# Kernel tuning notes

Measured on AMD Instinct MI355X. Metric: run time of the kernel, lower is better.

Reference implementation:

```python
import jax, jax.numpy as jnp
import numpy as np

B, N, FD = 8, 32768, 32
NUM_GROUP, GROUP_SIZE = 1024, 32
RAD_FIVE_DEG = 0.087266  # radians_of_five_degrees threshold


def setup_inputs() -> dict:
    key = jax.random.key(0)
    k1, k2, k3 = jax.random.split(key, 3)
    coord = jax.random.normal(k1, (B * N, 3), dtype=jnp.float32)
    feat = jax.random.normal(k2, (B * N, FD), dtype=jnp.float32)
    labels = jax.random.randint(k3, (B * N,), 0, 20)
    offset = jnp.cumsum(jnp.full((B,), N, dtype=jnp.int32))  # [N, 2N, ..., BN]
    return {"coord": coord, "feat": feat, "labels": labels, "offset": offset}


def _fps(coords, num_samples):
    """Farthest point sampling on one cloud. coords: [N,3] -> [num_samples] indices."""
    d = jnp.sum((coords - coords[0]) ** 2, axis=-1)  # dist to first selected point

    def step(dist, _):
        idx = jnp.argmax(dist)
        nd = jnp.sum((coords - coords[idx]) ** 2, axis=-1)
        return jnp.minimum(dist, nd), idx

    _, idxs = jax.lax.scan(step, d, None, length=num_samples - 1)
    return jnp.concatenate([jnp.zeros((1,), dtype=idxs.dtype), idxs])


def reference(coord, feat, labels, offset):
    b = offset.shape[0]
    n = coord.shape[0] // b
    c = coord.reshape(b, n, 3)        # [B,N,3]
    f = feat.reshape(b, n, FD)        # [B,N,FD]
    lab = labels.reshape(b, n)

    # --- FPS: num_group samples per cloud ---
    s_idx = jax.vmap(_fps, in_axes=(0, None))(c, NUM_GROUP)  # [B,G]

    s_xyz = jnp.take_along_axis(c, s_idx[..., None], axis=1)          # [B,G,3]
    s_feat = jnp.take_along_axis(f, s_idx[..., None], axis=1)         # [B,G,FD]
    s_labels = jnp.take_along_axis(lab, s_idx, axis=1)                # [B,G]

    # --- kNN within each cloud: [B,G,N] distance matrix, top-k smallest ---
    d2 = jnp.sum((s_xyz[:, :, None, :] - c[:, None, :, :]) ** 2, axis=-1)  # [B,G,N]
    _, n_idx = jax.lax.top_k(-d2, GROUP_SIZE)                              # [B,G,K] ascending distance

    # gather neighbor features: [B,G,K,FD]
    s_n_feat = jax.vmap(lambda fb, ib: fb[ib])(f, n_idx)

    # --- point curvature: 2*atan2(||a*|b| - |a|*b||, ||a*|b| + |a|*b||) ---
    a = s_feat[:, :, None, :]                                   # [B,G,1,FD]
    an = jnp.linalg.norm(a, axis=-1, keepdims=True)             # [B,G,1,1]
    bn = jnp.linalg.norm(s_n_feat, axis=-1, keepdims=True)      # [B,G,K,1]
    num = jnp.linalg.norm(a * bn - an * s_n_feat, axis=-1)      # [B,G,K]
    den = jnp.linalg.norm(a * bn + an * s_n_feat, axis=-1)      # [B,G,K]
    angles = 2.0 * jnp.arctan2(num, den)                        # [B,G,K]
    # drop self neighbor (first, distance 0), mean over remaining
    p_curv = jnp.mean(angles[:, :, 1:], axis=-1, keepdims=True)  # [B,G,1]

    shape_weight = (p_curv > RAD_FIVE_DEG).astype(jnp.int32).squeeze(-1)  # [B,G]
    feat_out = jnp.concatenate([s_feat, p_curv], axis=-1)                 # [B,G,FD+1]

    # flat index back to parent (global flat indexing, per original flat layout)
    s_idx_flat = s_idx + jnp.arange(b, dtype=s_idx.dtype)[:, None] * n

    return (s_xyz.reshape(-1, 3),
            feat_out.reshape(-1, FD + 1),
            shape_weight.reshape(-1),
            s_labels.reshape(-1),
            s_idx_flat.reshape(-1))
```

## Files before the change

### kernel.cpp

```cpp
#include <hip/hip_runtime.h>
#include <math.h>

#define BATCH   8
#define NPTS    32768
#define FDIM    32
#define NGROUP  1024
#define GSIZE   32
#define KLANE   8

#define NBLK    8
#define FTPB    512
#define CHUNK   (NPTS / NBLK)
#define NFPSBLK (BATCH * NBLK)
#define KNNQPB  8
#define NKNNBLK ((BATCH * NGROUP) / KNNQPB)

__device__ __forceinline__ float dist2f(float ax, float ay, float az,
                                        float bx, float by, float bz) {
  float dx = __fsub_rn(ax, bx);
  float dy = __fsub_rn(ay, by);
  float dz = __fsub_rn(az, bz);
  return __fadd_rn(__fadd_rn(__fmul_rn(dx, dx), __fmul_rn(dy, dy)),
                   __fmul_rn(dz, dz));
}

#define X8(M) M(0) M(1) M(2) M(3) M(4) M(5) M(6) M(7)

__global__ __launch_bounds__(FTPB) void fused_kernel(
    const float* __restrict__ coord, const float* __restrict__ feat,
    const int* __restrict__ labels,
    unsigned long long* __restrict__ slots,
    int* __restrict__ s_idx_ws,
    float* __restrict__ out) {
  __shared__ float redv[8];
  __shared__ int   redp[8];
  __shared__ unsigned long long bcast;

  const int bx   = blockIdx.x;
  const int tid  = threadIdx.x;
  const int lane = tid & 63;
  const int wid  = tid >> 6;

  if (bx < NFPSBLK) {
    const int b    = bx & 7;
    const int bk   = bx >> 3;
    const float* __restrict__ c = coord + (size_t)b * NPTS * 3;
    const float3* __restrict__ c3 = (const float3*)c;
    const int pbase = bk * CHUNK + tid;

#define DECL8(i) float x##i, y##i, z##i, d##i;
    X8(DECL8)
#undef DECL8

    float qx = c[0], qy = c[1], qz = c[2];
    float bestv = -1.0f; int bestp = 0;
#define LOAD8(i) { int p = pbase + (i) * FTPB; float3 v = c3[p];            \
    x##i = v.x; y##i = v.y; z##i = v.z;                                      \
    float t2 = dist2f(v.x, v.y, v.z, qx, qy, qz); d##i = t2;                 \
    if (t2 > bestv) { bestv = t2; bestp = p; } }
    X8(LOAD8)
#undef LOAD8

    if (bk == 0 && tid == 0)
      __hip_atomic_store(&s_idx_ws[b * NGROUP + 0], 1, __ATOMIC_RELAXED,
                         __HIP_MEMORY_SCOPE_AGENT);

    for (int t = 1; t < NGROUP; ++t) {
      float v = bestv; int p = bestp;
      #pragma unroll
      for (int m = 1; m < 64; m <<= 1) {
        float ov = __shfl_xor(v, m, 64);
        int   op = __shfl_xor(p, m, 64);
        if (ov > v || (ov == v && op < p)) { v = ov; p = op; }
      }
      if (lane == 0) { redv[wid] = v; redp[wid] = p; }
      __syncthreads();

      if (wid == 0) {
        float gv = redv[lane & 7]; int gp = redp[lane & 7];
        #pragma unroll
        for (int m = 1; m < 8; m <<= 1) {
          float ov = __shfl_xor(gv, m, 64);
          int   op = __shfl_xor(gp, m, 64);
          if (ov > gv || (ov == gv && op < gp)) { gv = ov; gp = op; }
        }
        unsigned long long* base = slots + (size_t)(t & 1) * (BATCH * NBLK);
        if (lane == 0) {
          unsigned long long pk = ((unsigned long long)t << 47)
                                | ((unsigned long long)__float_as_uint(gv) << 15)
                                | (unsigned long long)(0x7FFF - gp);
          __hip_atomic_store(base + (b << 3) + bk, pk, __ATOMIC_RELEASE,
                             __HIP_MEMORY_SCOPE_AGENT);
        }
        unsigned long long pk2 = 0;
        if (lane < 8) {
          const unsigned long long* sl = base + (b << 3) + lane;
          do {
            pk2 = __hip_atomic_load(sl, __ATOMIC_ACQUIRE,
                                    __HIP_MEMORY_SCOPE_AGENT);
          } while ((int)(pk2 >> 47) != t);
        }
        #pragma unroll
        for (int m = 1; m < 8; m <<= 1) {
          unsigned long long o = __shfl_xor(pk2, m, 64);
          if (o > pk2) pk2 = o;
        }
        if (lane == 0) bcast = pk2;
      }
      __syncthreads();

      const unsigned long long wpk = bcast;
      const int gp = 0x7FFF - (int)(wpk & 0x7FFF);
      if (bk == 0 && tid == 0)
        __hip_atomic_store(&s_idx_ws[b * NGROUP + t], gp + 1,
                           __ATOMIC_RELAXED, __HIP_MEMORY_SCOPE_AGENT);
      if (t == NGROUP - 1) break;

      float3 q = c3[gp];
      qx = q.x; qy = q.y; qz = q.z;
      bestv = -1.0f; bestp = 0;
#define UPD8(i) { float t2 = dist2f(x##i, y##i, z##i, qx, qy, qz);           \
    float nd = fminf(d##i, t2); d##i = nd;                                   \
    if (nd > bestv) { bestv = nd; bestp = pbase + (i) * FTPB; } }
      X8(UPD8)
#undef UPD8
    }
    return;
  }

  const int qid = (bx - NFPSBLK) * KNNQPB + wid;
  const int b   = qid >> 10;
  const float* __restrict__ c = coord + (size_t)b * NPTS * 3;

  const int tq = qid & (NGROUP - 1);
  int enc = __hip_atomic_load(&s_idx_ws[qid], __ATOMIC_RELAXED,
                              __HIP_MEMORY_SCOPE_AGENT);
  for (int i = tq >> 2; i > 0 && enc == 0; --i) {
    __builtin_amdgcn_s_sleep(127);
    enc = __hip_atomic_load(&s_idx_ws[qid], __ATOMIC_RELAXED,
                            __HIP_MEMORY_SCOPE_AGENT);
  }
  while (enc == 0) {
    __builtin_amdgcn_s_sleep(64);
    enc = __hip_atomic_load(&s_idx_ws[qid], __ATOMIC_RELAXED,
                            __HIP_MEMORY_SCOPE_AGENT);
  }
  const int sp = __builtin_amdgcn_readfirstlane(enc - 1);
  const int gq = b * NPTS + sp;
  const float qx = coord[(size_t)gq * 3 + 0];
  const float qy = coord[(size_t)gq * 3 + 1];
  const float qz = coord[(size_t)gq * 3 + 2];

  float lv[KLANE]; int li[KLANE];
  #pragma unroll
  for (int j = 0; j < KLANE; ++j) { lv[j] = 1e30f; li[j] = 0x7fffffff; }

#define INSERT(D2, P) \
  if ((D2) < lv[KLANE - 1]) { \
    _Pragma("unroll") \
    for (int j = KLANE - 1; j >= 1; --j) { \
      bool up = (D2) < lv[j - 1]; \
      float nv = up ? lv[j - 1] : (((D2) < lv[j]) ? (D2) : lv[j]); \
      int   ni = up ? li[j - 1] : (((D2) < lv[j]) ? (P)  : li[j]); \
      lv[j] = nv; li[j] = ni; \
    } \
    if ((D2) < lv[0]) { lv[0] = (D2); li[0] = (P); } \
  }

  for (int s = 0; s < NPTS / 256; ++s) {
    int p = (s << 8) | (lane << 2);
    const float4* c4 = (const float4*)(c + (size_t)p * 3);
    float4 f0 = c4[0], f1 = c4[1], f2 = c4[2];
    float dA = dist2f(f0.x, f0.y, f0.z, qx, qy, qz);
    float dB = dist2f(f0.w, f1.x, f1.y, qx, qy, qz);
    float dC = dist2f(f1.z, f1.w, f2.x, qx, qy, qz);
    float dD = dist2f(f2.y, f2.z, f2.w, qx, qy, qz);
    INSERT(dA, p);
    INSERT(dB, p + 1);
    INSERT(dC, p + 2);
    INSERT(dD, p + 3);
  }
#undef INSERT

  int nbp = 0;
  for (int r = 0; r < GSIZE; ++r) {
    float mv = lv[0]; int mp = li[0];
    #pragma unroll
    for (int m = 1; m < 64; m <<= 1) {
      float ov = __shfl_xor(mv, m, 64);
      int   op = __shfl_xor(mp, m, 64);
      if (ov < mv || (ov == mv && op < mp)) { mv = ov; mp = op; }
    }
    if (lane == r) nbp = mp;
    if (lv[0] == mv && li[0] == mp) {
      #pragma unroll
      for (int j = 0; j < KLANE - 1; ++j) { lv[j] = lv[j + 1]; li[j] = li[j + 1]; }
      lv[KLANE - 1] = 1e30f; li[KLANE - 1] = 0x7fffffff;
    }
  }

  const float* aRow = feat + (size_t)gq * FDIM;
  float my_a = (lane < FDIM) ? aRow[lane] : 0.0f;

  float ang = 0.0f;
  if (lane >= 1 && lane < GSIZE) {
    const float4* a4 = (const float4*)aRow;
    const float4* b4 = (const float4*)(feat + ((size_t)b * NPTS + nbp) * FDIM);
    float4 av[FDIM / 4], bv[FDIM / 4];
    float aa = 0.0f, bb = 0.0f;
    #pragma unroll
    for (int k = 0; k < FDIM / 4; ++k) {
      av[k] = a4[k]; bv[k] = b4[k];
      aa += av[k].x * av[k].x + av[k].y * av[k].y + av[k].z * av[k].z + av[k].w * av[k].w;
      bb += bv[k].x * bv[k].x + bv[k].y * bv[k].y + bv[k].z * bv[k].z + bv[k].w * bv[k].w;
    }
    float an = sqrtf(aa), bn = sqrtf(bb);
    float num2 = 0.0f, den2 = 0.0f;
    #pragma unroll
    for (int k = 0; k < FDIM / 4; ++k) {
      float n0 = av[k].x * bn - an * bv[k].x, dd0 = av[k].x * bn + an * bv[k].x;
      float n1 = av[k].y * bn - an * bv[k].y, dd1 = av[k].y * bn + an * bv[k].y;
      float n2 = av[k].z * bn - an * bv[k].z, dd2 = av[k].z * bn + an * bv[k].z;
      float n3 = av[k].w * bn - an * bv[k].w, dd3 = av[k].w * bn + an * bv[k].w;
      num2 += n0 * n0 + n1 * n1 + n2 * n2 + n3 * n3;
      den2 += dd0 * dd0 + dd1 * dd1 + dd2 * dd2 + dd3 * dd3;
    }
    ang = 2.0f * atan2f(sqrtf(num2), sqrtf(den2));
  }

  float tot = ang;
  #pragma unroll
  for (int m = 1; m < 64; m <<= 1) tot += __shfl_xor(tot, m, 64);
  float p_curv = tot / 31.0f;

  float* out_xyz  = out;
  float* out_feat = out + (size_t)BATCH * NGROUP * 3;
  float* out_sw   = out_feat + (size_t)BATCH * NGROUP * (FDIM + 1);
  float* out_lab  = out_sw  + (size_t)BATCH * NGROUP;
  float* out_sif  = out_lab + (size_t)BATCH * NGROUP;

  if (lane < FDIM)  out_feat[(size_t)qid * (FDIM + 1) + lane] = my_a;
  if (lane == FDIM) out_feat[(size_t)qid * (FDIM + 1) + FDIM] = p_curv;
  if (lane == 0) {
    out_xyz[(size_t)qid * 3 + 0] = qx;
    out_xyz[(size_t)qid * 3 + 1] = qy;
    out_xyz[(size_t)qid * 3 + 2] = qz;
    out_sw[qid]  = (p_curv > 0.087266f) ? 1.0f : 0.0f;
    out_lab[qid] = (float)labels[gq];
    out_sif[qid] = (float)gq;
  }
}

extern "C" void kernel_launch(void* const* d_in, const int* in_sizes, int n_in,
                              void* d_out, int out_size, void* d_ws, size_t ws_size,
                              hipStream_t stream) {
  const float* coord  = (const float*)d_in[0];
  const float* feat   = (const float*)d_in[1];
  const int*   labels = (const int*)d_in[2];

  unsigned long long* slots = (unsigned long long*)d_ws;
  int* s_idx_ws = (int*)((char*)d_ws +
                         2 * BATCH * NBLK * sizeof(unsigned long long));
  const size_t zbytes = 2 * BATCH * NBLK * sizeof(unsigned long long)
                      + (size_t)BATCH * NGROUP * sizeof(int);

  hipMemsetAsync(d_ws, 0, zbytes, stream);
  fused_kernel<<<NFPSBLK + NKNNBLK, FTPB, 0, stream>>>(
      coord, feat, labels, slots, s_idx_ws, (float*)d_out);
}
```

Baseline: 2.872 ms.

## Split FPS per cloud over two blocks with pairwise slot exchange

Farthest point sampling now splits each cloud over 2 blocks instead of 8, so each thread holds 32 points in registers rather than 8. The cross-block exchange becomes a two-party handshake with slots padded onto separate cache lines. Launch bounds now request 2 blocks per CU, and the kNN wait loop sleeps for a shorter initial period. The aim is to cut the latency of the inter-block sync on every FPS step, which dominates the sequential loop, at the cost of 4x more distance work per thread per step and higher register pressure.

```diff
diff --git a/kernel.cpp b/kernel.cpp
--- a/kernel.cpp
+++ b/kernel.cpp
@@ -8,10 +8,12 @@
 #define GSIZE   32
 #define KLANE   8
 
-#define NBLK    8
+#define NBLK    2
 #define FTPB    512
 #define CHUNK   (NPTS / NBLK)
+#define PPT     (CHUNK / FTPB)
 #define NFPSBLK (BATCH * NBLK)
+#define SLOTSTR 8
 #define KNNQPB  8
 #define NKNNBLK ((BATCH * NGROUP) / KNNQPB)
 
@@ -24,9 +26,7 @@
                    __fmul_rn(dz, dz));
 }
 
-#define X8(M) M(0) M(1) M(2) M(3) M(4) M(5) M(6) M(7)
-
-__global__ __launch_bounds__(FTPB) void fused_kernel(
+__global__ __launch_bounds__(FTPB, 2) void fused_kernel(
     const float* __restrict__ coord, const float* __restrict__ feat,
     const int* __restrict__ labels,
     unsigned long long* __restrict__ slots,
@@ -48,25 +48,26 @@
     const float3* __restrict__ c3 = (const float3*)c;
     const int pbase = bk * CHUNK + tid;
 
-#define DECL8(i) float x##i, y##i, z##i, d##i;
-    X8(DECL8)
-#undef DECL8
+    float px[PPT], py[PPT], pz[PPT], pd[PPT];
 
     float qx = c[0], qy = c[1], qz = c[2];
-    float bestv = -1.0f; int bestp = 0;
-#define LOAD8(i) { int p = pbase + (i) * FTPB; float3 v = c3[p];            \
-    x##i = v.x; y##i = v.y; z##i = v.z;                                      \
-    float t2 = dist2f(v.x, v.y, v.z, qx, qy, qz); d##i = t2;                 \
-    if (t2 > bestv) { bestv = t2; bestp = p; } }
-    X8(LOAD8)
-#undef LOAD8
+    float bestv = -1.0f; int besti = 0;
+    #pragma unroll
+    for (int i = 0; i < PPT; ++i) {
+      int p = pbase + i * FTPB;
+      float3 v = c3[p];
+      px[i] = v.x; py[i] = v.y; pz[i] = v.z;
+      float t2 = dist2f(v.x, v.y, v.z, qx, qy, qz);
+      pd[i] = t2;
+      if (t2 > bestv) { bestv = t2; besti = i; }
+    }
 
     if (bk == 0 && tid == 0)
       __hip_atomic_store(&s_idx_ws[b * NGROUP + 0], 1, __ATOMIC_RELAXED,
                          __HIP_MEMORY_SCOPE_AGENT);
 
     for (int t = 1; t < NGROUP; ++t) {
-      float v = bestv; int p = bestp;
+      float v = bestv; int p = pbase + (besti << 9);
       #pragma unroll
       for (int m = 1; m < 64; m <<= 1) {
         float ov = __shfl_xor(v, m, 64);
@@ -84,46 +85,42 @@
           int   op = __shfl_xor(gp, m, 64);
           if (ov > gv || (ov == gv && op < gp)) { gv = ov; gp = op; }
         }
-        unsigned long long* base = slots + (size_t)(t & 1) * (BATCH * NBLK);
         if (lane == 0) {
-          unsigned long long pk = ((unsigned long long)t << 47)
-                                | ((unsigned long long)__float_as_uint(gv) << 15)
-                                | (unsigned long long)(0x7FFF - gp);
-          __hip_atomic_store(base + (b << 3) + bk, pk, __ATOMIC_RELEASE,
-                             __HIP_MEMORY_SCOPE_AGENT);
+          unsigned long long* base =
+              slots + (size_t)(t & 1) * (BATCH * NBLK * SLOTSTR);
+          unsigned long long own = ((unsigned long long)t << 47)
+                                 | ((unsigned long long)__float_as_uint(gv) << 15)
+                                 | (unsigned long long)(0x7FFF - gp);
+          __hip_atomic_store(base + (b * NBLK + bk) * SLOTSTR, own,
+                             __ATOMIC_RELEASE, __HIP_MEMORY_SCOPE_AGENT);
+          const unsigned long long* rs = base + (b * NBLK + (bk ^ 1)) * SLOTSTR;
+          unsigned long long rem;
+          do {
+            rem = __hip_atomic_load(rs, __ATOMIC_ACQUIRE,
+                                    __HIP_MEMORY_SCOPE_AGENT);
+          } while ((int)(rem >> 47) != t);
+          bcast = (rem > own) ? rem : own;
         }
-        unsigned long long pk2 = 0;
-        if (lane < 8) {
-          const unsigned long long* sl = base + (b << 3) + lane;
-          do {
-            pk2 = __hip_atomic_load(sl, __ATOMIC_ACQUIRE,
-                                    __HIP_MEMORY_SCOPE_AGENT);
-          } while ((int)(pk2 >> 47) != t);
-        }
-        #pragma unroll
-        for (int m = 1; m < 8; m <<= 1) {
-          unsigned long long o = __shfl_xor(pk2, m, 64);
-          if (o > pk2) pk2 = o;
-        }
-        if (lane == 0) bcast = pk2;
       }
       __syncthreads();
 
       const unsigned long long wpk = bcast;
-      const int gp = 0x7FFF - (int)(wpk & 0x7FFF);
+      const int gsel = 0x7FFF - (int)(wpk & 0x7FFF);
       if (bk == 0 && tid == 0)
-        __hip_atomic_store(&s_idx_ws[b * NGROUP + t], gp + 1,
+        __hip_atomic_store(&s_idx_ws[b * NGROUP + t], gsel + 1,
                            __ATOMIC_RELAXED, __HIP_MEMORY_SCOPE_AGENT);
       if (t == NGROUP - 1) break;
 
-      float3 q = c3[gp];
+      float3 q = c3[gsel];
       qx = q.x; qy = q.y; qz = q.z;
-      bestv = -1.0f; bestp = 0;
-#define UPD8(i) { float t2 = dist2f(x##i, y##i, z##i, qx, qy, qz);           \
-    float nd = fminf(d##i, t2); d##i = nd;                                   \
-    if (nd > bestv) { bestv = nd; bestp = pbase + (i) * FTPB; } }
-      X8(UPD8)
-#undef UPD8
+      bestv = -1.0f; besti = 0;
+      #pragma unroll
+      for (int i = 0; i < PPT; ++i) {
+        float t2 = dist2f(px[i], py[i], pz[i], qx, qy, qz);
+        float nd = fminf(pd[i], t2);
+        pd[i] = nd;
+        if (nd > bestv) { bestv = nd; besti = i; }
+      }
     }
     return;
   }
@@ -135,7 +132,7 @@
   const int tq = qid & (NGROUP - 1);
   int enc = __hip_atomic_load(&s_idx_ws[qid], __ATOMIC_RELAXED,
                               __HIP_MEMORY_SCOPE_AGENT);
-  for (int i = tq >> 2; i > 0 && enc == 0; --i) {
+  for (int i = tq >> 3; i > 0 && enc == 0; --i) {
     __builtin_amdgcn_s_sleep(127);
     enc = __hip_atomic_load(&s_idx_ws[qid], __ATOMIC_RELAXED,
                             __HIP_MEMORY_SCOPE_AGENT);
@@ -260,8 +257,8 @@
 
   unsigned long long* slots = (unsigned long long*)d_ws;
   int* s_idx_ws = (int*)((char*)d_ws +
-                         2 * BATCH * NBLK * sizeof(unsigned long long));
-  const size_t zbytes = 2 * BATCH * NBLK * sizeof(unsigned long long)
+                         2 * BATCH * NBLK * SLOTSTR * sizeof(unsigned long long));
+  const size_t zbytes = 2 * BATCH * NBLK * SLOTSTR * sizeof(unsigned long long)
                       + (size_t)BATCH * NGROUP * sizeof(int);
 
   hipMemsetAsync(d_ws, 0, zbytes, stream);
```

After: 3.238 ms. 12.7% more time.

## Halve FPS blocks per cloud, pad sync slots, shorten kNN backoff

Applied to the files above, without the earlier changes.

Each cloud's farthest-point sampling now runs on 4 cooperating blocks instead of 8, so each thread holds 16 points in registers and fewer blocks take part in the cross-block argmax exchange on every step. The per-block slots are padded to a stride of 8 words so that each block writes to its own cache line, avoiding false sharing while others poll. The kNN blocks' initial sleep-wait loop is also shortened. The trade-off is double the distance-update work per thread on each step and higher register pressure, exchanged for lower synchronization latency and fewer occupied CUs.

```diff
diff --git a/kernel.cpp b/kernel.cpp
--- a/kernel.cpp
+++ b/kernel.cpp
@@ -8,10 +8,12 @@
 #define GSIZE   32
 #define KLANE   8
 
-#define NBLK    8
+#define NBLK    4
 #define FTPB    512
 #define CHUNK   (NPTS / NBLK)
+#define PPT     (CHUNK / FTPB)
 #define NFPSBLK (BATCH * NBLK)
+#define SLOTSTR 8
 #define KNNQPB  8
 #define NKNNBLK ((BATCH * NGROUP) / KNNQPB)
 
@@ -24,7 +26,8 @@
                    __fmul_rn(dz, dz));
 }
 
-#define X8(M) M(0) M(1) M(2) M(3) M(4) M(5) M(6) M(7)
+#define X16(M) M(0) M(1) M(2) M(3) M(4) M(5) M(6) M(7) \
+               M(8) M(9) M(10) M(11) M(12) M(13) M(14) M(15)
 
 __global__ __launch_bounds__(FTPB) void fused_kernel(
     const float* __restrict__ coord, const float* __restrict__ feat,
@@ -48,18 +51,18 @@
     const float3* __restrict__ c3 = (const float3*)c;
     const int pbase = bk * CHUNK + tid;
 
-#define DECL8(i) float x##i, y##i, z##i, d##i;
-    X8(DECL8)
-#undef DECL8
+#define DECL16(i) float x##i, y##i, z##i, d##i;
+    X16(DECL16)
+#undef DECL16
 
     float qx = c[0], qy = c[1], qz = c[2];
     float bestv = -1.0f; int bestp = 0;
-#define LOAD8(i) { int p = pbase + (i) * FTPB; float3 v = c3[p];            \
+#define LOAD16(i) { int p = pbase + (i) * FTPB; float3 v = c3[p];            \
     x##i = v.x; y##i = v.y; z##i = v.z;                                      \
     float t2 = dist2f(v.x, v.y, v.z, qx, qy, qz); d##i = t2;                 \
     if (t2 > bestv) { bestv = t2; bestp = p; } }
-    X8(LOAD8)
-#undef LOAD8
+    X16(LOAD16)
+#undef LOAD16
 
     if (bk == 0 && tid == 0)
       __hip_atomic_store(&s_idx_ws[b * NGROUP + 0], 1, __ATOMIC_RELAXED,
@@ -84,24 +87,25 @@
           int   op = __shfl_xor(gp, m, 64);
           if (ov > gv || (ov == gv && op < gp)) { gv = ov; gp = op; }
         }
-        unsigned long long* base = slots + (size_t)(t & 1) * (BATCH * NBLK);
+        unsigned long long* base =
+            slots + (size_t)(t & 1) * (BATCH * NBLK * SLOTSTR);
         if (lane == 0) {
-          unsigned long long pk = ((unsigned long long)t << 47)
-                                | ((unsigned long long)__float_as_uint(gv) << 15)
-                                | (unsigned long long)(0x7FFF - gp);
-          __hip_atomic_store(base + (b << 3) + bk, pk, __ATOMIC_RELEASE,
-                             __HIP_MEMORY_SCOPE_AGENT);
+          unsigned long long own = ((unsigned long long)t << 47)
+                                 | ((unsigned long long)__float_as_uint(gv) << 15)
+                                 | (unsigned long long)(0x7FFF - gp);
+          __hip_atomic_store(base + (b * NBLK + bk) * SLOTSTR, own,
+                             __ATOMIC_RELEASE, __HIP_MEMORY_SCOPE_AGENT);
         }
         unsigned long long pk2 = 0;
-        if (lane < 8) {
-          const unsigned long long* sl = base + (b << 3) + lane;
+        if (lane < NBLK) {
+          const unsigned long long* sl = base + (b * NBLK + lane) * SLOTSTR;
           do {
             pk2 = __hip_atomic_load(sl, __ATOMIC_ACQUIRE,
                                     __HIP_MEMORY_SCOPE_AGENT);
           } while ((int)(pk2 >> 47) != t);
         }
         #pragma unroll
-        for (int m = 1; m < 8; m <<= 1) {
+        for (int m = 1; m < NBLK; m <<= 1) {
           unsigned long long o = __shfl_xor(pk2, m, 64);
           if (o > pk2) pk2 = o;
         }
@@ -110,20 +114,20 @@
       __syncthreads();
 
       const unsigned long long wpk = bcast;
-      const int gp = 0x7FFF - (int)(wpk & 0x7FFF);
+      const int gsel = 0x7FFF - (int)(wpk & 0x7FFF);
       if (bk == 0 && tid == 0)
-        __hip_atomic_store(&s_idx_ws[b * NGROUP + t], gp + 1,
+        __hip_atomic_store(&s_idx_ws[b * NGROUP + t], gsel + 1,
                            __ATOMIC_RELAXED, __HIP_MEMORY_SCOPE_AGENT);
       if (t == NGROUP - 1) break;
 
-      float3 q = c3[gp];
+      float3 q = c3[gsel];
       qx = q.x; qy = q.y; qz = q.z;
       bestv = -1.0f; bestp = 0;
-#define UPD8(i) { float t2 = dist2f(x##i, y##i, z##i, qx, qy, qz);           \
+#define UPD16(i) { float t2 = dist2f(x##i, y##i, z##i, qx, qy, qz);          \
     float nd = fminf(d##i, t2); d##i = nd;                                   \
     if (nd > bestv) { bestv = nd; bestp = pbase + (i) * FTPB; } }
-      X8(UPD8)
-#undef UPD8
+      X16(UPD16)
+#undef UPD16
     }
     return;
   }
@@ -135,7 +139,7 @@
   const int tq = qid & (NGROUP - 1);
   int enc = __hip_atomic_load(&s_idx_ws[qid], __ATOMIC_RELAXED,
                               __HIP_MEMORY_SCOPE_AGENT);
-  for (int i = tq >> 2; i > 0 && enc == 0; --i) {
+  for (int i = tq >> 3; i > 0 && enc == 0; --i) {
     __builtin_amdgcn_s_sleep(127);
     enc = __hip_atomic_load(&s_idx_ws[qid], __ATOMIC_RELAXED,
                             __HIP_MEMORY_SCOPE_AGENT);
@@ -260,8 +264,8 @@
 
   unsigned long long* slots = (unsigned long long*)d_ws;
   int* s_idx_ws = (int*)((char*)d_ws +
-                         2 * BATCH * NBLK * sizeof(unsigned long long));
-  const size_t zbytes = 2 * BATCH * NBLK * sizeof(unsigned long long)
+                         2 * BATCH * NBLK * SLOTSTR * sizeof(unsigned long long));
+  const size_t zbytes = 2 * BATCH * NBLK * SLOTSTR * sizeof(unsigned long long)
                       + (size_t)BATCH * NGROUP * sizeof(int);
 
   hipMemsetAsync(d_ws, 0, zbytes, stream);
```

New measurement: 2.750 ms. 1.04x faster.
